# Kernel optimization log

Measured on AMD Instinct MI355X. Metric: run time of the kernel, lower is better.

The kernel has to match this reference:

```python
import jax, jax.numpy as jnp
import numpy as np

ENCODER_DIM, DECODER_DIM, ATTN_DIM = 2048, 512, 512
B, P = 128, 196  # batch, num_pixels (14x14)


def setup_inputs() -> dict:
    key = jax.random.key(0)
    ks = jax.random.split(key, 8)
    s_e = 1.0 / np.sqrt(ENCODER_DIM)
    s_d = 1.0 / np.sqrt(DECODER_DIM)
    s_a = 1.0 / np.sqrt(ATTN_DIM)
    return {
        "encoder_out": jax.random.normal(ks[0], (B, P, ENCODER_DIM), jnp.float32),
        "decoder_hidden": jax.random.normal(ks[1], (B, DECODER_DIM), jnp.float32),
        "W_enc": jax.random.uniform(ks[2], (ENCODER_DIM, ATTN_DIM), jnp.float32, -s_e, s_e),
        "b_enc": jax.random.uniform(ks[3], (ATTN_DIM,), jnp.float32, -s_e, s_e),
        "W_dec": jax.random.uniform(ks[4], (DECODER_DIM, ATTN_DIM), jnp.float32, -s_d, s_d),
        "b_dec": jax.random.uniform(ks[5], (ATTN_DIM,), jnp.float32, -s_d, s_d),
        "W_full": jax.random.uniform(ks[6], (ATTN_DIM,), jnp.float32, -s_a, s_a),
        "b_full": jax.random.uniform(ks[7], (), jnp.float32, -s_a, s_a),
    }


def reference(encoder_out, decoder_hidden, W_enc, b_enc, W_dec, b_dec, W_full, b_full):
    # att1: [B, P, A]; att2: [B, A]
    att1 = jnp.einsum("bpe,ea->bpa", encoder_out, W_enc) + b_enc
    att2 = decoder_hidden @ W_dec + b_dec
    # broadcast add + relu + score projection -> [B, P]
    att = jax.nn.relu(att1 + att2[:, None, :]) @ W_full + b_full
    alpha = jax.nn.softmax(att, axis=1)  # over pixels
    # weighted sum over pixels -> [B, E]
    attention_weighted_encoding = jnp.einsum("bpe,bp->be", encoder_out, alpha)
    return (attention_weighted_encoding, alpha)
```

## Files before the change

kernel.cpp:

```cpp
#include <hip/hip_runtime.h>
#include <hip/hip_bf16.h>

#define ENC_DIM 2048
#define DEC_DIM 512
#define ATT_DIM 512
#define BATCH   128
#define NPIX    196
#define NROWS   (BATCH * NPIX)

typedef short bf16x8 __attribute__((ext_vector_type(8)));
typedef float f32x4  __attribute__((ext_vector_type(4)));
typedef unsigned short u16x8 __attribute__((ext_vector_type(8)));

__device__ __forceinline__ unsigned short f2bf(float f) {
    union { float f; unsigned u; } v; v.f = f;
    unsigned r = v.u + 0x7fffu + ((v.u >> 16) & 1u);
    return (unsigned short)(r >> 16);
}

__device__ __forceinline__ void gload16(const void* g, void* l) {
    __builtin_amdgcn_global_load_lds(
        (const __attribute__((address_space(1))) unsigned int*)g,
        (__attribute__((address_space(3))) unsigned int*)l, 16, 0, 0);
}

__global__ void k0_transpose(const float* __restrict__ W_enc,
                             unsigned short* __restrict__ Wt) {
    __shared__ float ts[64][65];
    const int a0 = blockIdx.x * 64;
    const int e0 = blockIdx.y * 64;
    const int tx = threadIdx.x & 15;
    const int ty = threadIdx.x >> 4;
    #pragma unroll
    for (int p = 0; p < 4; ++p) {
        const int e = ty + p * 16;
        const float4 v = *(const float4*)&W_enc[(size_t)(e0 + e) * ATT_DIM + a0 + tx * 4];
        ts[e][tx * 4 + 0] = v.x; ts[e][tx * 4 + 1] = v.y;
        ts[e][tx * 4 + 2] = v.z; ts[e][tx * 4 + 3] = v.w;
    }
    __syncthreads();
    #pragma unroll
    for (int p = 0; p < 4; ++p) {
        const int a = ty + p * 16;
        ushort4 u;
        u.x = f2bf(ts[tx * 4 + 0][a]);
        u.y = f2bf(ts[tx * 4 + 1][a]);
        u.z = f2bf(ts[tx * 4 + 2][a]);
        u.w = f2bf(ts[tx * 4 + 3][a]);
        *(ushort4*)&Wt[(size_t)(a0 + a) * ENC_DIM + e0 + tx * 4] = u;
    }
}

__global__ void k1_att2(const float* __restrict__ dh, const float* __restrict__ W_dec,
                        const float* __restrict__ b_dec, const float* __restrict__ b_enc,
                        const float* __restrict__ b_full,
                        float* __restrict__ att2, float* __restrict__ att) {
    __shared__ float dhs[DEC_DIM];
    const int b = blockIdx.x, t = threadIdx.x;
    dhs[t]       = dh[b * DEC_DIM + t];
    dhs[t + 256] = dh[b * DEC_DIM + t + 256];
    __syncthreads();
    float acc0 = 0.f, acc1 = 0.f;
    for (int d = 0; d < DEC_DIM; ++d) {
        const float h = dhs[d];
        acc0 += h * W_dec[d * ATT_DIM + t];
        acc1 += h * W_dec[d * ATT_DIM + t + 256];
    }
    att2[b * ATT_DIM + t]       = acc0 + b_dec[t]       + b_enc[t];
    att2[b * ATT_DIM + t + 256] = acc1 + b_dec[t + 256] + b_enc[t + 256];
    const int gid = b * 256 + t;
    if (gid < NROWS) att[gid] = b_full[0];
}

__launch_bounds__(256, 3)
__global__ void k2_gemm(const float* __restrict__ enc, const unsigned short* __restrict__ Wt,
                        const float* __restrict__ att2, const float* __restrict__ W_full,
                        float* __restrict__ att) {
    __shared__ __align__(16) unsigned short As[128 * 72];
    __shared__ __align__(16) unsigned short Bs[128 * 64];
    __shared__ float att2s[2][128];
    __shared__ float wfs[128];

    const int t = threadIdx.x;
    const int tile = (blockIdx.x & 7) * 98 + (blockIdx.x >> 3);
    const int n0   = (tile & 3) * 128;
    const int row0 = (tile >> 2) * 128;
    const int b0   = row0 / NPIX;
    const int rows_left = (b0 + 1) * NPIX - row0;

    if (t < 128) {
        att2s[0][t] = att2[b0 * ATT_DIM + n0 + t];
        att2s[1][t] = (b0 + 1 < BATCH) ? att2[(b0 + 1) * ATT_DIM + n0 + t] : 0.f;
        wfs[t]      = W_full[n0 + t];
    }

    const int w    = t >> 6;
    const int lane = t & 63;
    const int q    = lane >> 4;
    const int cl   = lane & 15;
    const int wm   = (w >> 1) * 64;
    const int wn   = (w & 1) * 64;

    f32x4 acc[4][4] = {};

    const int ar = t >> 3;
    const int ak = (t & 7) * 8;
    const float* encA = enc + (size_t)(row0 + ar) * ENC_DIM + ak;

    const int br = lane >> 3;
    const int bc = ((lane & 7) ^ br) * 8;
    const unsigned short* WtB = Wt + (size_t)(n0 + w * 32 + br) * ENC_DIM + bc;

    for (int kk = 0; kk < ENC_DIM; kk += 64) {
        __syncthreads();
        #pragma unroll
        for (int i = 0; i < 4; ++i)
            gload16(WtB + (size_t)i * 8 * ENC_DIM + kk,
                    &Bs[(w * 32 + i * 8) * 64]);
        #pragma unroll
        for (int p = 0; p < 4; ++p) {
            const float4 v0 = *(const float4*)(encA + (size_t)p * 32 * ENC_DIM + kk);
            const float4 v1 = *(const float4*)(encA + (size_t)p * 32 * ENC_DIM + kk + 4);
            u16x8 u;
            u[0] = f2bf(v0.x); u[1] = f2bf(v0.y); u[2] = f2bf(v0.z); u[3] = f2bf(v0.w);
            u[4] = f2bf(v1.x); u[5] = f2bf(v1.y); u[6] = f2bf(v1.z); u[7] = f2bf(v1.w);
            *(u16x8*)&As[(ar + p * 32) * 72 + ak] = u;
        }
        __syncthreads();

        #pragma unroll
        for (int h = 0; h < 2; ++h) {
            bf16x8 af[4], bfr[4];
            #pragma unroll
            for (int i = 0; i < 4; ++i)
                af[i]  = *(const bf16x8*)&As[(wm + i * 16 + cl) * 72 + h * 32 + q * 8];
            #pragma unroll
            for (int i = 0; i < 4; ++i)
                bfr[i] = *(const bf16x8*)&Bs[(wn + i * 16 + cl) * 64
                                             + (((h * 4 + q) ^ (cl & 7)) * 8)];
            #pragma unroll
            for (int mi = 0; mi < 4; ++mi)
                #pragma unroll
                for (int ni = 0; ni < 4; ++ni)
                    acc[mi][ni] = __builtin_amdgcn_mfma_f32_16x16x32_bf16(
                        af[mi], bfr[ni], acc[mi][ni], 0, 0, 0);
        }
    }

    #pragma unroll
    for (int mi = 0; mi < 4; ++mi) {
        float rs[4];
        #pragma unroll
        for (int i = 0; i < 4; ++i) {
            const int lr  = wm + mi * 16 + q * 4 + i;
            const int sel = (lr >= rows_left) ? 1 : 0;
            float sum = 0.f;
            #pragma unroll
            for (int ni = 0; ni < 4; ++ni) {
                const int j = wn + ni * 16 + cl;
                float v = acc[mi][ni][i] + att2s[sel][j];
                v = fmaxf(v, 0.f);
                sum += v * wfs[j];
            }
            rs[i] = sum;
        }
        #pragma unroll
        for (int o = 1; o < 16; o <<= 1) {
            #pragma unroll
            for (int i = 0; i < 4; ++i) rs[i] += __shfl_xor(rs[i], o);
        }
        if (cl == 0) {
            #pragma unroll
            for (int i = 0; i < 4; ++i) {
                const int r = row0 + wm + mi * 16 + q * 4 + i;
                atomicAdd(&att[r], rs[i]);
            }
        }
    }
}

__global__ void k3_softmax(float* __restrict__ att_alpha) {
    __shared__ float red[4];
    const int b = blockIdx.x, t = threadIdx.x;
    const int w = t >> 6, lane = t & 63;
    const float x = (t < NPIX) ? att_alpha[b * NPIX + t] : -INFINITY;
    float m = x;
    #pragma unroll
    for (int o = 32; o >= 1; o >>= 1) m = fmaxf(m, __shfl_xor(m, o));
    if (lane == 0) red[w] = m;
    __syncthreads();
    m = fmaxf(fmaxf(red[0], red[1]), fmaxf(red[2], red[3]));
    const float e = (t < NPIX) ? __expf(x - m) : 0.f;
    float s = e;
    #pragma unroll
    for (int o = 32; o >= 1; o >>= 1) s += __shfl_xor(s, o);
    __syncthreads();
    if (lane == 0) red[w] = s;
    __syncthreads();
    s = red[0] + red[1] + red[2] + red[3];
    if (t < NPIX) att_alpha[b * NPIX + t] = e / s;
}

__global__ void k4_awe(const float* __restrict__ enc, const float* __restrict__ alpha,
                       float* __restrict__ awe) {
    __shared__ float as[NPIX];
    const int b  = blockIdx.y;
    const int t  = threadIdx.x;
    const int e0 = blockIdx.x * 512 + t * 4;
    as[t] = alpha[b * NPIX + t];
    if (t < NPIX - 128) as[t + 128] = alpha[b * NPIX + t + 128];
    __syncthreads();
    const float* base = enc + (size_t)b * NPIX * ENC_DIM + e0;
    f32x4 a[8] = {};
    for (int p = 0; p < 192; p += 8) {
        #pragma unroll
        for (int j = 0; j < 8; ++j) {
            const f32x4 v = *(const f32x4*)(base + (size_t)(p + j) * ENC_DIM);
            a[j] += as[p + j] * v;
        }
    }
    #pragma unroll
    for (int j = 0; j < 4; ++j) {
        const f32x4 v = *(const f32x4*)(base + (size_t)(192 + j) * ENC_DIM);
        a[j] += as[192 + j] * v;
    }
    const f32x4 r = ((a[0] + a[1]) + (a[2] + a[3])) + ((a[4] + a[5]) + (a[6] + a[7]));
    *(f32x4*)&awe[(size_t)b * ENC_DIM + e0] = r;
}

extern "C" void kernel_launch(void* const* d_in, const int* in_sizes, int n_in,
                              void* d_out, int out_size, void* d_ws, size_t ws_size,
                              hipStream_t stream) {
    const float* enc    = (const float*)d_in[0];
    const float* dh     = (const float*)d_in[1];
    const float* W_enc  = (const float*)d_in[2];
    const float* b_enc  = (const float*)d_in[3];
    const float* W_dec  = (const float*)d_in[4];
    const float* b_dec  = (const float*)d_in[5];
    const float* W_full = (const float*)d_in[6];
    const float* b_full = (const float*)d_in[7];

    float* awe   = (float*)d_out;
    float* alpha = awe + BATCH * ENC_DIM;

    unsigned short* Wt   = (unsigned short*)d_ws;
    float*          att2 = (float*)((char*)d_ws + (size_t)ATT_DIM * ENC_DIM * 2);

    k0_transpose<<<dim3(8, 32),  256, 0, stream>>>(W_enc, Wt);
    k1_att2     <<<128,          256, 0, stream>>>(dh, W_dec, b_dec, b_enc, b_full, att2, alpha);
    k2_gemm     <<<784,          256, 0, stream>>>(enc, Wt, att2, W_full, alpha);
    k3_softmax  <<<128,          256, 0, stream>>>(alpha);
    k4_awe      <<<dim3(4, 128), 128, 0, stream>>>(enc, alpha, awe);
}
```

Measured before the change: 436.1 us.

## Load fp32 A tiles via direct-to-LDS, fuse softmax into weighted-sum kernel

The GEMM now streams fp32 encoder tiles straight into shared memory with async global-to-LDS loads using a swizzled layout, converting to bf16 when fragments are read, instead of converting in registers before the LDS store. The softmax kernel is merged into the weighted-sum kernel, which recomputes softmax per block and splits the pixel reduction across four waves with an LDS reduction, using more blocks. The att2 kernel is split across twice as many blocks. This doubles A-tile LDS footprint and repeats bf16 conversion per fragment read, and the softmax is recomputed redundantly in every column block.

```diff
diff --git a/kernel.cpp b/kernel.cpp
--- a/kernel.cpp
+++ b/kernel.cpp
@@ -16,6 +16,12 @@
     union { float f; unsigned u; } v; v.f = f;
     unsigned r = v.u + 0x7fffu + ((v.u >> 16) & 1u);
     return (unsigned short)(r >> 16);
+}
+
+__device__ __forceinline__ short bfc(float f) {
+    union { __hip_bfloat16 h; short s; } v;
+    v.h = __float2bfloat16(f);
+    return v.s;
 }
 
 __device__ __forceinline__ void gload16(const void* g, void* l) {
@@ -54,30 +60,31 @@
 __global__ void k1_att2(const float* __restrict__ dh, const float* __restrict__ W_dec,
                         const float* __restrict__ b_dec, const float* __restrict__ b_enc,
                         const float* __restrict__ b_full,
-                        float* __restrict__ att2, float* __restrict__ att) {
+                        float* __restrict__ att2, float* __restrict__ score) {
     __shared__ float dhs[DEC_DIM];
-    const int b = blockIdx.x, t = threadIdx.x;
+    const int bid = blockIdx.x, t = threadIdx.x;
+    const int b = bid >> 1;
+    const int c = (bid & 1) * 256 + t;
     dhs[t]       = dh[b * DEC_DIM + t];
     dhs[t + 256] = dh[b * DEC_DIM + t + 256];
     __syncthreads();
     float acc0 = 0.f, acc1 = 0.f;
-    for (int d = 0; d < DEC_DIM; ++d) {
-        const float h = dhs[d];
-        acc0 += h * W_dec[d * ATT_DIM + t];
-        acc1 += h * W_dec[d * ATT_DIM + t + 256];
-    }
-    att2[b * ATT_DIM + t]       = acc0 + b_dec[t]       + b_enc[t];
-    att2[b * ATT_DIM + t + 256] = acc1 + b_dec[t + 256] + b_enc[t + 256];
-    const int gid = b * 256 + t;
-    if (gid < NROWS) att[gid] = b_full[0];
+    #pragma unroll 8
+    for (int d = 0; d < 256; ++d) {
+        acc0 += dhs[d]       * W_dec[d * ATT_DIM + c];
+        acc1 += dhs[d + 256] * W_dec[(d + 256) * ATT_DIM + c];
+    }
+    att2[b * ATT_DIM + c] = acc0 + acc1 + b_dec[c] + b_enc[c];
+    const int gid = bid * 256 + t;
+    if (gid < NROWS) score[gid] = b_full[0];
 }
 
 __launch_bounds__(256, 3)
 __global__ void k2_gemm(const float* __restrict__ enc, const unsigned short* __restrict__ Wt,
                         const float* __restrict__ att2, const float* __restrict__ W_full,
-                        float* __restrict__ att) {
-    __shared__ __align__(16) unsigned short As[128 * 72];
-    __shared__ __align__(16) unsigned short Bs[128 * 64];
+                        float* __restrict__ score) {
+    __shared__ __align__(16) float          Asf[128 * 64];
+    __shared__ __align__(16) unsigned short Bs [128 * 64];
     __shared__ float att2s[2][128];
     __shared__ float wfs[128];
 
@@ -103,28 +110,34 @@
 
     f32x4 acc[4][4] = {};
 
-    const int ar = t >> 3;
-    const int ak = (t & 7) * 8;
-    const float* encA = enc + (size_t)(row0 + ar) * ENC_DIM + ak;
+    const int r4 = lane >> 4;
+    const int sl = lane & 15;
+    const float* aS0 = enc + (size_t)(row0 + w * 32 + r4)     * ENC_DIM + ((sl ^ r4)       << 2);
+    const float* aS1 = enc + (size_t)(row0 + w * 32 + 4 + r4) * ENC_DIM + ((sl ^ (4 + r4)) << 2);
 
     const int br = lane >> 3;
     const int bc = ((lane & 7) ^ br) * 8;
     const unsigned short* WtB = Wt + (size_t)(n0 + w * 32 + br) * ENC_DIM + bc;
 
+    unsigned ab[4], ab2[4];
+    #pragma unroll
+    for (int mi = 0; mi < 4; ++mi) {
+        unsigned base = ((unsigned)(wm + mi * 16 + cl) << 8) + ((unsigned)(cl & 7) << 4);
+        base ^= (unsigned)(q << 5);
+        ab[mi]  = base;
+        ab2[mi] = base ^ 16u;
+    }
+    const char* Ab = (const char*)Asf;
+
     for (int kk = 0; kk < ENC_DIM; kk += 64) {
         __syncthreads();
         #pragma unroll
         for (int i = 0; i < 4; ++i)
-            gload16(WtB + (size_t)i * 8 * ENC_DIM + kk,
-                    &Bs[(w * 32 + i * 8) * 64]);
-        #pragma unroll
-        for (int p = 0; p < 4; ++p) {
-            const float4 v0 = *(const float4*)(encA + (size_t)p * 32 * ENC_DIM + kk);
-            const float4 v1 = *(const float4*)(encA + (size_t)p * 32 * ENC_DIM + kk + 4);
-            u16x8 u;
-            u[0] = f2bf(v0.x); u[1] = f2bf(v0.y); u[2] = f2bf(v0.z); u[3] = f2bf(v0.w);
-            u[4] = f2bf(v1.x); u[5] = f2bf(v1.y); u[6] = f2bf(v1.z); u[7] = f2bf(v1.w);
-            *(u16x8*)&As[(ar + p * 32) * 72 + ak] = u;
+            gload16(WtB + (size_t)i * 8 * ENC_DIM + kk, &Bs[(w * 32 + i * 8) * 64]);
+        #pragma unroll
+        for (int i = 0; i < 4; ++i) {
+            gload16(aS0 + (size_t)i * 8 * ENC_DIM + kk, &Asf[(w * 32 + i * 8)     * 64]);
+            gload16(aS1 + (size_t)i * 8 * ENC_DIM + kk, &Asf[(w * 32 + i * 8 + 4) * 64]);
         }
         __syncthreads();
 
@@ -132,8 +145,14 @@
         for (int h = 0; h < 2; ++h) {
             bf16x8 af[4], bfr[4];
             #pragma unroll
-            for (int i = 0; i < 4; ++i)
-                af[i]  = *(const bf16x8*)&As[(wm + i * 16 + cl) * 72 + h * 32 + q * 8];
+            for (int mi = 0; mi < 4; ++mi) {
+                const f32x4 fa = *(const f32x4*)(Ab + ab[mi]  + h * 128);
+                const f32x4 fb = *(const f32x4*)(Ab + ab2[mi] + h * 128);
+                bf16x8 u;
+                u[0] = bfc(fa[0]); u[1] = bfc(fa[1]); u[2] = bfc(fa[2]); u[3] = bfc(fa[3]);
+                u[4] = bfc(fb[0]); u[5] = bfc(fb[1]); u[6] = bfc(fb[2]); u[7] = bfc(fb[3]);
+                af[mi] = u;
+            }
             #pragma unroll
             for (int i = 0; i < 4; ++i)
                 bfr[i] = *(const bf16x8*)&Bs[(wn + i * 16 + cl) * 64
@@ -173,21 +192,25 @@
             #pragma unroll
             for (int i = 0; i < 4; ++i) {
                 const int r = row0 + wm + mi * 16 + q * 4 + i;
-                atomicAdd(&att[r], rs[i]);
+                atomicAdd(&score[r], rs[i]);
             }
         }
     }
 }
 
-__global__ void k3_softmax(float* __restrict__ att_alpha) {
+__global__ void k4_awe(const float* __restrict__ enc, const float* __restrict__ score,
+                       float* __restrict__ alpha, float* __restrict__ awe) {
+    __shared__ float as[NPIX];
     __shared__ float red[4];
-    const int b = blockIdx.x, t = threadIdx.x;
-    const int w = t >> 6, lane = t & 63;
-    const float x = (t < NPIX) ? att_alpha[b * NPIX + t] : -INFINITY;
+    __shared__ f32x4 redv[4][64];
+    const int b  = blockIdx.y;
+    const int t  = threadIdx.x;
+    const int wv = t >> 6, lane = t & 63;
+    const float x = (t < NPIX) ? score[b * NPIX + t] : -INFINITY;
     float m = x;
     #pragma unroll
     for (int o = 32; o >= 1; o >>= 1) m = fmaxf(m, __shfl_xor(m, o));
-    if (lane == 0) red[w] = m;
+    if (lane == 0) red[wv] = m;
     __syncthreads();
     m = fmaxf(fmaxf(red[0], red[1]), fmaxf(red[2], red[3]));
     const float e = (t < NPIX) ? __expf(x - m) : 0.f;
@@ -195,37 +218,33 @@
     #pragma unroll
     for (int o = 32; o >= 1; o >>= 1) s += __shfl_xor(s, o);
     __syncthreads();
-    if (lane == 0) red[w] = s;
+    if (lane == 0) red[wv] = s;
     __syncthreads();
     s = red[0] + red[1] + red[2] + red[3];
-    if (t < NPIX) att_alpha[b * NPIX + t] = e / s;
-}
-
-__global__ void k4_awe(const float* __restrict__ enc, const float* __restrict__ alpha,
-                       float* __restrict__ awe) {
-    __shared__ float as[NPIX];
-    const int b  = blockIdx.y;
-    const int t  = threadIdx.x;
-    const int e0 = blockIdx.x * 512 + t * 4;
-    as[t] = alpha[b * NPIX + t];
-    if (t < NPIX - 128) as[t + 128] = alpha[b * NPIX + t + 128];
-    __syncthreads();
+    const float a = e / s;
+    if (t < NPIX) {
+        as[t] = a;
+        if (blockIdx.x == 0) alpha[b * NPIX + t] = a;
+    }
+    __syncthreads();
+    const int e0 = blockIdx.x * 256 + lane * 4;
     const float* base = enc + (size_t)b * NPIX * ENC_DIM + e0;
-    f32x4 a[8] = {};
-    for (int p = 0; p < 192; p += 8) {
-        #pragma unroll
-        for (int j = 0; j < 8; ++j) {
-            const f32x4 v = *(const f32x4*)(base + (size_t)(p + j) * ENC_DIM);
-            a[j] += as[p + j] * v;
-        }
-    }
-    #pragma unroll
-    for (int j = 0; j < 4; ++j) {
-        const f32x4 v = *(const f32x4*)(base + (size_t)(192 + j) * ENC_DIM);
-        a[j] += as[192 + j] * v;
-    }
-    const f32x4 r = ((a[0] + a[1]) + (a[2] + a[3])) + ((a[4] + a[5]) + (a[6] + a[7]));
-    *(f32x4*)&awe[(size_t)b * ENC_DIM + e0] = r;
+    f32x4 a0 = {}, a1 = {}, a2 = {}, a3 = {};
+    int p = wv;
+    #pragma unroll 4
+    for (int it = 0; it < 12; ++it, p += 16) {
+        a0 += as[p]      * *(const f32x4*)(base + (size_t)(p)      * ENC_DIM);
+        a1 += as[p + 4]  * *(const f32x4*)(base + (size_t)(p + 4)  * ENC_DIM);
+        a2 += as[p + 8]  * *(const f32x4*)(base + (size_t)(p + 8)  * ENC_DIM);
+        a3 += as[p + 12] * *(const f32x4*)(base + (size_t)(p + 12) * ENC_DIM);
+    }
+    a0 += as[p] * *(const f32x4*)(base + (size_t)p * ENC_DIM);
+    redv[wv][lane] = (a0 + a1) + (a2 + a3);
+    __syncthreads();
+    if (wv == 0) {
+        const f32x4 r = (redv[0][lane] + redv[1][lane]) + (redv[2][lane] + redv[3][lane]);
+        *(f32x4*)&awe[(size_t)b * ENC_DIM + e0] = r;
+    }
 }
 
 extern "C" void kernel_launch(void* const* d_in, const int* in_sizes, int n_in,
@@ -243,12 +262,12 @@
     float* awe   = (float*)d_out;
     float* alpha = awe + BATCH * ENC_DIM;
 
-    unsigned short* Wt   = (unsigned short*)d_ws;
-    float*          att2 = (float*)((char*)d_ws + (size_t)ATT_DIM * ENC_DIM * 2);
+    unsigned short* Wt    = (unsigned short*)d_ws;
+    float*          att2  = (float*)((char*)d_ws + (size_t)ATT_DIM * ENC_DIM * 2);
+    float*          score = att2 + (size_t)BATCH * ATT_DIM;
 
     k0_transpose<<<dim3(8, 32),  256, 0, stream>>>(W_enc, Wt);
-    k1_att2     <<<128,          256, 0, stream>>>(dh, W_dec, b_dec, b_enc, b_full, att2, alpha);
-    k2_gemm     <<<784,          256, 0, stream>>>(enc, Wt, att2, W_full, alpha);
-    k3_softmax  <<<128,          256, 0, stream>>>(alpha);
-    k4_awe      <<<dim3(4, 128), 128, 0, stream>>>(enc, alpha, awe);
-}
+    k1_att2     <<<256,          256, 0, stream>>>(dh, W_dec, b_dec, b_enc, b_full, att2, score);
+    k2_gemm     <<<784,          256, 0, stream>>>(enc, Wt, att2, W_full, score);
+    k4_awe      <<<dim3(8, 128), 256, 0, stream>>>(enc, score, alpha, awe);
+}
```

After: 396.1 us. 9.2% less time.
